# Optimization experiments

Hardware: AMD Instinct MI355X
Metric: run time of the kernel (lower is better)

Reference implementation:

```python
import jax, jax.numpy as jnp
import numpy as np

NHEAD = 8
TEMP = 1.0
LAMB = 1.0
G_MIN = 1e-3


def _linear(x, w, b):
    # torch nn.Linear convention: w is (out, in)
    return x @ w.T + b


def _ln(x, s, b):
    m = x.mean(-1, keepdims=True)
    v = ((x - m) ** 2).mean(-1, keepdims=True)
    return (x - m) / jnp.sqrt(v + 1e-5) * s + b


def _gate(x, w, b):
    # UncertaintyGate, gate_mode='mu_times_evi'
    nig = _linear(x, w, b)  # [B, L, 4]
    mu = nig[..., 0]
    v = jax.nn.softplus(nig[..., 1]) + 1e-6
    alpha = jax.nn.softplus(nig[..., 2]) + 1.0 + 1e-6
    beta = jax.nn.softplus(nig[..., 3]) + 1e-6
    sigma_e2 = beta / (v * (alpha - 1.0))
    g = jax.nn.sigmoid(mu) * jnp.exp(-LAMB * sigma_e2)
    return jnp.clip(g, G_MIN, 1.0)  # [B, L]


def _cross_attn(q, k, v, gate, mask):
    B, Lq, D = q.shape
    Lk = k.shape[1]
    hd = D // NHEAD
    q = q.reshape(B, Lq, NHEAD, hd).transpose(0, 2, 1, 3)
    k = k.reshape(B, Lk, NHEAD, hd).transpose(0, 2, 1, 3)
    v = v.reshape(B, Lk, NHEAD, hd).transpose(0, 2, 1, 3)
    scores = jnp.einsum('bhqd,bhkd->bhqk', q, k) / jnp.sqrt(jnp.float32(hd))
    scores = scores + jnp.log(gate + 1e-9)[:, None, None, :]  # per-key log-gate bias
    scores = jnp.where(mask[:, None, None, :] == 0, -1e9, scores)
    attn = jax.nn.softmax(scores / TEMP, axis=-1)
    out = jnp.einsum('bhqk,bhkd->bhqd', attn, v)
    return out.transpose(0, 2, 1, 3).reshape(B, Lq, D)


def _ffn(x, w1, b1, w2, b2):
    return _linear(jax.nn.gelu(_linear(x, w1, b1), approximate=False), w2, b2)


def setup_inputs() -> dict:
    key = jax.random.key(0)
    ks = iter(jax.random.split(key, 64))
    D, B, Ld, Lp = 512, 16, 256, 1024
    def w(shape, s=0.02):
        return jax.random.normal(next(ks), shape, jnp.float32) * s
    inp = {
        'h_d': jax.random.normal(next(ks), (B, Ld, D), jnp.float32),
        'h_p': jax.random.normal(next(ks), (B, Lp, D), jnp.float32),
        'gd_w': w((4, D)), 'gd_b': jnp.zeros((4,), jnp.float32),
        'gp_w': w((4, D)), 'gp_b': jnp.zeros((4,), jnp.float32),
        'wqd_w': w((D, D)), 'wqd_b': jnp.zeros((D,), jnp.float32),
        'wkp_w': w((D, D)), 'wkp_b': jnp.zeros((D,), jnp.float32),
        'wvp_w': w((D, D)), 'wvp_b': jnp.zeros((D,), jnp.float32),
        'wqp_w': w((D, D)), 'wqp_b': jnp.zeros((D,), jnp.float32),
        'wkd_w': w((D, D)), 'wkd_b': jnp.zeros((D,), jnp.float32),
        'wvd_w': w((D, D)), 'wvd_b': jnp.zeros((D,), jnp.float32),
        'od_w': w((D, D)), 'od_b': jnp.zeros((D,), jnp.float32),
        'op_w': w((D, D)), 'op_b': jnp.zeros((D,), jnp.float32),
        'fd1_w': w((4 * D, D)), 'fd1_b': jnp.zeros((4 * D,), jnp.float32),
        'fd2_w': w((D, 4 * D)), 'fd2_b': jnp.zeros((D,), jnp.float32),
        'fp1_w': w((4 * D, D)), 'fp1_b': jnp.zeros((4 * D,), jnp.float32),
        'fp2_w': w((D, 4 * D)), 'fp2_b': jnp.zeros((D,), jnp.float32),
        'nd1_s': jnp.ones((D,), jnp.float32), 'nd1_b': jnp.zeros((D,), jnp.float32),
        'nd2_s': jnp.ones((D,), jnp.float32), 'nd2_b': jnp.zeros((D,), jnp.float32),
        'np1_s': jnp.ones((D,), jnp.float32), 'np1_b': jnp.zeros((D,), jnp.float32),
        'np2_s': jnp.ones((D,), jnp.float32), 'np2_b': jnp.zeros((D,), jnp.float32),
        'mask_d': jnp.ones((B, Ld), jnp.int32),
        'mask_p': jnp.ones((B, Lp), jnp.int32),
    }
    return inp


def reference(h_d, h_p, gd_w, gd_b, gp_w, gp_b, wqd_w, wqd_b, wkp_w, wkp_b,
              wvp_w, wvp_b, wqp_w, wqp_b, wkd_w, wkd_b, wvd_w, wvd_b,
              od_w, od_b, op_w, op_b, fd1_w, fd1_b, fd2_w, fd2_b,
              fp1_w, fp1_b, fp2_w, fp2_b, nd1_s, nd1_b, nd2_s, nd2_b,
              np1_s, np1_b, np2_s, np2_b, mask_d, mask_p):
    # gates are computed from the ORIGINAL inputs
    g_d = _gate(h_d, gd_w, gd_b)
    g_p = _gate(h_p, gp_w, gp_b)
    # drug attends to protein
    attn_d = _cross_attn(_linear(h_d, wqd_w, wqd_b),
                         _linear(h_p, wkp_w, wkp_b),
                         _linear(h_p, wvp_w, wvp_b), g_p, mask_p)
    h_d = _ln(h_d + _linear(attn_d, od_w, od_b), nd1_s, nd1_b)
    # protein attends to UPDATED drug (matches original control flow)
    attn_p = _cross_attn(_linear(h_p, wqp_w, wqp_b),
                         _linear(h_d, wkd_w, wkd_b),
                         _linear(h_d, wvd_w, wvd_b), g_d, mask_d)
    h_p = _ln(h_p + _linear(attn_p, op_w, op_b), np1_s, np1_b)
    h_d = _ln(h_d + _ffn(h_d, fd1_w, fd1_b, fd2_w, fd2_b), nd2_s, nd2_b)
    h_p = _ln(h_p + _ffn(h_p, fp1_w, fp1_b, fp2_w, fp2_b), np2_s, np2_b)
    return (h_d, h_p)
```

## Files before the change

kernel.cpp:

```cpp
#include <hip/hip_runtime.h>

typedef float f32x4 __attribute__((ext_vector_type(4)));
typedef short bfrag __attribute__((ext_vector_type(8)));
typedef short s16x8 __attribute__((ext_vector_type(8)));
typedef unsigned short u16;

__device__ __forceinline__ u16 f2bf(float f) {
  union { float f; unsigned u; } x; x.f = f;
  unsigned r = x.u + 0x7fffu + ((x.u >> 16) & 1u);
  return (u16)(r >> 16);
}
__device__ __forceinline__ float bf2f(u16 v) {
  union { unsigned u; float f; } x; x.u = ((unsigned)v) << 16;
  return x.f;
}

__device__ __forceinline__ void g2l16(const void* g, void* l) {
  void* gnc = const_cast<void*>(g);
  __builtin_amdgcn_global_load_lds((__attribute__((address_space(1))) void*)gnc,
                                   (__attribute__((address_space(3))) void*)l, 16, 0, 0);
}

__device__ __forceinline__ f32x4 mfma16(bfrag a, bfrag b, f32x4 c) {
  asm volatile("v_mfma_f32_16x16x32_bf16 %0, %1, %2, %0" : "+v"(c) : "v"(a), "v"(b));
  return c;
}

__device__ __forceinline__ float wred_sum(float s) {
  #pragma unroll
  for (int o = 32; o; o >>= 1) s += __shfl_xor(s, o);
  return s;
}

__device__ __forceinline__ float gelu_f(float v) {
  return 0.5f * v * (1.f + erff(v * 0.70710678118f));
}

struct CvtArgs {
  const float* s[14];
  u16* d[14];
  int eb[14];
};

__global__ __launch_bounds__(256) void cvt_all(CvtArgs a) {
  const int blk = blockIdx.x;
  int base = 0;
  const float* sp = a.s[0];
  u16* dp = a.d[0];
  #pragma unroll
  for (int i = 0; i < 13; ++i) {
    if (blk >= a.eb[i]) { base = a.eb[i]; sp = a.s[i + 1]; dp = a.d[i + 1]; }
  }
  const size_t gi = ((size_t)(blk - base) * 256 + threadIdx.x) * 4;
  float4 f = *(const float4*)(sp + gi);
  ushort4 o;
  o.x = f2bf(f.x); o.y = f2bf(f.y); o.z = f2bf(f.z); o.w = f2bf(f.w);
  *(ushort4*)(dp + gi) = o;
}

__global__ __launch_bounds__(512) void biascat_k(
    const float* __restrict__ bkp, const float* __restrict__ bvp,
    const float* __restrict__ bqp, const float* __restrict__ bkd,
    const float* __restrict__ bvd, float* __restrict__ bp3,
    float* __restrict__ bd2) {
  int t = threadIdx.x;
  bp3[t] = bkp[t];
  bp3[512 + t] = bvp[t];
  bp3[1024 + t] = bqp[t];
  bd2[t] = bkd[t];
  bd2[512 + t] = bvd[t];
}

__device__ __forceinline__ float softplus_s(float x) {
  return fmaxf(x, 0.f) + log1pf(expf(-fabsf(x)));
}

__global__ __launch_bounds__(256) void gate_k(
    const float* __restrict__ hd, const float* __restrict__ hp,
    const float* __restrict__ wd, const float* __restrict__ bd,
    const float* __restrict__ wp, const float* __restrict__ bp,
    float* __restrict__ lgd, float* __restrict__ lgp, int mdTok) {
  const int lane = threadIdx.x & 63, wv = threadIdx.x >> 6;
  size_t tok = (size_t)blockIdx.x * 4 + wv;
  const float* h; const float* w4; const float* b4; float* lg;
  if (tok < (size_t)mdTok) { h = hd; w4 = wd; b4 = bd; lg = lgd; }
  else { h = hp; w4 = wp; b4 = bp; lg = lgp; tok -= mdTok; }
  const float* x = h + tok * 512;
  float s0 = 0.f, s1 = 0.f, s2 = 0.f, s3 = 0.f;
  #pragma unroll
  for (int i = 0; i < 8; ++i) {
    int c = (i << 6) + lane;
    float xv = x[c];
    s0 += xv * w4[c];
    s1 += xv * w4[512 + c];
    s2 += xv * w4[1024 + c];
    s3 += xv * w4[1536 + c];
  }
  s0 = wred_sum(s0); s1 = wred_sum(s1); s2 = wred_sum(s2); s3 = wred_sum(s3);
  if (lane == 0) {
    float mu = s0 + b4[0];
    float va = softplus_s(s1 + b4[1]) + 1e-6f;
    float al = softplus_s(s2 + b4[2]) + 1.f + 1e-6f;
    float be = softplus_s(s3 + b4[3]) + 1e-6f;
    float se2 = be / (va * (al - 1.f));
    float g = (1.f / (1.f + expf(-mu))) * expf(-se2);
    g = fminf(fmaxf(g, 1e-3f), 1.f);
    lg[tok] = logf(g + 1e-9f);
  }
}

__device__ __forceinline__ void ln_body(const u16* res, const u16* y,
                                        const float* sc, const float* bi,
                                        void* outv, int fp32out, size_t row,
                                        int lane) {
  const int c0 = lane * 8;
  float v[8];
  s16x8 yv = *(const s16x8*)(y + row * 512 + c0);
  s16x8 rv = *(const s16x8*)(res + row * 512 + c0);
  float s = 0.f;
  #pragma unroll
  for (int i = 0; i < 8; ++i) {
    v[i] = bf2f((u16)rv[i]) + bf2f((u16)yv[i]);
    s += v[i];
  }
  s = wred_sum(s);
  float m = s * (1.f / 512.f);
  float s2 = 0.f;
  #pragma unroll
  for (int i = 0; i < 8; ++i) { float d = v[i] - m; s2 += d * d; }
  s2 = wred_sum(s2);
  float inv = rsqrtf(s2 * (1.f / 512.f) + 1e-5f);
  float4 sc0 = *(const float4*)(sc + c0), sc1 = *(const float4*)(sc + c0 + 4);
  float4 bi0 = *(const float4*)(bi + c0), bi1 = *(const float4*)(bi + c0 + 4);
  float scv[8] = {sc0.x, sc0.y, sc0.z, sc0.w, sc1.x, sc1.y, sc1.z, sc1.w};
  float biv[8] = {bi0.x, bi0.y, bi0.z, bi0.w, bi1.x, bi1.y, bi1.z, bi1.w};
  float o[8];
  #pragma unroll
  for (int i = 0; i < 8; ++i) o[i] = (v[i] - m) * inv * scv[i] + biv[i];
  if (fp32out) {
    float* of = (float*)outv + row * 512 + c0;
    *(float4*)of = float4{o[0], o[1], o[2], o[3]};
    *(float4*)(of + 4) = float4{o[4], o[5], o[6], o[7]};
  } else {
    s16x8 ov;
    #pragma unroll
    for (int i = 0; i < 8; ++i) ov[i] = (short)f2bf(o[i]);
    *(s16x8*)((u16*)outv + row * 512 + c0) = ov;
  }
}

__global__ __launch_bounds__(256) void ln_k(const u16* __restrict__ res,
                                            const u16* __restrict__ y,
                                            const float* __restrict__ sc,
                                            const float* __restrict__ bi,
                                            u16* __restrict__ out) {
  const int lane = threadIdx.x & 63, w = threadIdx.x >> 6;
  const size_t row = (size_t)blockIdx.x * 4 + w;
  ln_body(res, y, sc, bi, out, 0, row, lane);
}

__global__ __launch_bounds__(256) void lnf_k(
    const u16* __restrict__ rd, const u16* __restrict__ yd,
    const float* __restrict__ scd, const float* __restrict__ bid,
    float* __restrict__ od,
    const u16* __restrict__ rp, const u16* __restrict__ yp,
    const float* __restrict__ scp, const float* __restrict__ bip,
    float* __restrict__ op, int mdRows) {
  const int lane = threadIdx.x & 63, w = threadIdx.x >> 6;
  size_t row = (size_t)blockIdx.x * 4 + w;
  if (row < (size_t)mdRows)
    ln_body(rd, yd, scd, bid, od, 1, row, lane);
  else
    ln_body(rp, yp, scp, bip, op, 1, row - mdRows, lane);
}

template <int KT>
__global__ __launch_bounds__(256) void flash_k(
    const u16* __restrict__ Q, const u16* __restrict__ Kv,
    const u16* __restrict__ Vt, const float* __restrict__ logg,
    const int* __restrict__ mask, u16* __restrict__ Out,
    int Lq, int Lk, float scale) {
  __shared__ __align__(16) u16 Kl[KT * 64];
  __shared__ __align__(16) u16 Vl[64 * KT];
  __shared__ __align__(16) u16 Pl[64 * (KT + 8)];
  const int tid = threadIdx.x;
  const int lane = tid & 63, wv = tid >> 6;
  const int lr = lane & 15, lg4 = lane >> 4;
  const int bh = blockIdx.z;
  const int b = bh >> 3, h = bh & 7;
  const int q0 = blockIdx.x * 64;

  bfrag af[2];
  {
    const u16* qrow = Q + (size_t)(b * Lq + q0 + wv * 16 + lr) * 512 + h * 64;
    af[0] = *(const bfrag*)(qrow + lg4 * 8);
    af[1] = *(const bfrag*)(qrow + 32 + lg4 * 8);
  }
  float mreg[4] = {-3e38f, -3e38f, -3e38f, -3e38f};
  float lreg[4] = {0.f, 0.f, 0.f, 0.f};
  f32x4 Oa[4] = {};
  const float* lgb = logg + (size_t)b * Lk;
  const int* mkb = mask + (size_t)b * Lk;

  const int NKT = Lk / KT;
  for (int t = 0; t < NKT; ++t) {
    const int k0 = t * KT;
    __syncthreads();
    {
      const char* kb = (const char*)(Kv + (size_t)(b * Lk + k0) * 512 + h * 64);
      #pragma unroll
      for (int r = 0; r < KT / 32; ++r) {
        int o = r * 4096 + tid * 16;
        int rr = o >> 7, cd = (o >> 4) & 7;
        int cs = cd ^ (rr & 7);
        g2l16(kb + (size_t)rr * 1024 + cs * 16, (char*)Kl + o);
      }
      const char* vb = (const char*)(Vt + (size_t)bh * 64 * Lk + k0);
      #pragma unroll
      for (int r = 0; r < KT / 32; ++r) {
        int o = r * 4096 + tid * 16;
        int rr = o >> 8, cd = (o >> 4) & 15;
        int cs = (cd & 8) | ((cd & 7) ^ (rr & 7));
        g2l16(vb + (size_t)rr * (Lk * 2) + cs * 16, (char*)Vl + o);
      }
    }
    __syncthreads();

    f32x4 sa[KT / 16];
    #pragma unroll
    for (int n = 0; n < KT / 16; ++n) {
      sa[n] = f32x4{0.f, 0.f, 0.f, 0.f};
      int row = n * 16 + lr;
      #pragma unroll
      for (int ks = 0; ks < 2; ++ks) {
        bfrag kf = *(const bfrag*)(Kl + row * 64 + (((ks * 4 + lg4) ^ (row & 7)) * 8));
        sa[n] = mfma16(af[ks], kf, sa[n]);
      }
    }
    asm volatile("s_nop 7\n\ts_nop 7");

    float pv[KT / 16][4];
    float nm[4] = {-3e38f, -3e38f, -3e38f, -3e38f};
    #pragma unroll
    for (int n = 0; n < KT / 16; ++n) {
      int kk = k0 + n * 16 + lr;
      float lgv = lgb[kk];
      int mkv = mkb[kk];
      #pragma unroll
      for (int e = 0; e < 4; ++e) {
        float tv = mkv ? fmaf(sa[n][e], scale, lgv) : -1e9f;
        pv[n][e] = tv;
        nm[e] = fmaxf(nm[e], tv);
      }
    }
    float fac[4], rs[4];
    #pragma unroll
    for (int e = 0; e < 4; ++e) {
      nm[e] = fmaxf(nm[e], __shfl_xor(nm[e], 1));
      nm[e] = fmaxf(nm[e], __shfl_xor(nm[e], 2));
      nm[e] = fmaxf(nm[e], __shfl_xor(nm[e], 4));
      nm[e] = fmaxf(nm[e], __shfl_xor(nm[e], 8));
      nm[e] = fmaxf(nm[e], mreg[e]);
      fac[e] = __expf(mreg[e] - nm[e]);
      mreg[e] = nm[e];
      rs[e] = 0.f;
    }
    #pragma unroll
    for (int n = 0; n < KT / 16; ++n)
      #pragma unroll
      for (int e = 0; e < 4; ++e) {
        float p = __expf(pv[n][e] - nm[e]);
        pv[n][e] = p;
        rs[e] += p;
      }
    #pragma unroll
    for (int e = 0; e < 4; ++e) {
      rs[e] += __shfl_xor(rs[e], 1);
      rs[e] += __shfl_xor(rs[e], 2);
      rs[e] += __shfl_xor(rs[e], 4);
      rs[e] += __shfl_xor(rs[e], 8);
      lreg[e] = lreg[e] * fac[e] + rs[e];
    }
    #pragma unroll
    for (int n2 = 0; n2 < 4; ++n2)
      #pragma unroll
      for (int e = 0; e < 4; ++e) Oa[n2][e] *= fac[e];

    {
      int prow = wv * 16 + lg4 * 4;
      #pragma unroll
      for (int n = 0; n < KT / 16; ++n)
        #pragma unroll
        for (int e = 0; e < 4; ++e)
          Pl[(prow + e) * (KT + 8) + n * 16 + lr] = f2bf(pv[n][e]);
    }
    #pragma unroll
    for (int ks = 0; ks < KT / 32; ++ks) {
      bfrag pf = *(const bfrag*)(Pl + (wv * 16 + lr) * (KT + 8) + (ks * 4 + lg4) * 8);
      #pragma unroll
      for (int n2 = 0; n2 < 4; ++n2) {
        int vrow = n2 * 16 + lr;
        int ch = ks * 4 + lg4;
        int chs = (ch & 8) | ((ch & 7) ^ (vrow & 7));
        bfrag vf = *(const bfrag*)(Vl + vrow * KT + chs * 8);
        Oa[n2] = mfma16(pf, vf, Oa[n2]);
      }
    }
  }
  asm volatile("s_nop 7\n\ts_nop 7");

  float inv[4];
  #pragma unroll
  for (int e = 0; e < 4; ++e) inv[e] = 1.f / lreg[e];
  u16* ob = Out + (size_t)(b * Lq + q0 + wv * 16 + lg4 * 4) * 512 + h * 64;
  #pragma unroll
  for (int n2 = 0; n2 < 4; ++n2)
    #pragma unroll
    for (int e = 0; e < 4; ++e)
      ob[(size_t)e * 512 + n2 * 16 + lr] = f2bf(Oa[n2][e] * inv[e]);
}

struct GemmDesc {
  const u16* A;
  const u16* W;
  const float* bias;
  u16 *C, *C2, *C3;
  int K, lda, ldw, ldc, NB, TR, epi, nblocks;
};

__global__ __launch_bounds__(256) void gemm_k(GemmDesc d0, GemmDesc d1) {
  __shared__ __align__(16) u16 Al[128 * 32];
  __shared__ __align__(16) u16 Wl[128 * 32];
  const int tid = threadIdx.x;
  const int qq = gridDim.x >> 3;
  int wg = (blockIdx.x & 7) * qq + (blockIdx.x >> 3);
  const GemmDesc& d = (wg < d0.nblocks) ? d0 : d1;
  if (wg >= d0.nblocks) wg -= d0.nblocks;
  const int bx = wg % d.NB, by = wg / d.NB;
  const int row0 = by * 128, col0 = bx * 128;
  const int lane = tid & 63, wv = tid >> 6;
  const int wr = wv >> 1, wc = wv & 1;
  const int rowW = wr * 64, colW = wc * 64;
  const int lr = lane & 15, lg4 = lane >> 4;
  const int K = d.K;

  const u16* aSrc[2];
  const u16* wSrc[2];
  int aDst[2], wDst[2];
  #pragma unroll
  for (int r = 0; r < 2; ++r) {
    int o = r * 4096 + tid * 16;
    int row = o >> 6, cd = (o >> 4) & 3, cs = cd ^ ((row >> 1) & 3);
    aSrc[r] = d.A + (size_t)(row0 + row) * d.lda + cs * 8;
    wSrc[r] = d.W + (size_t)(col0 + row) * d.ldw + cs * 8;
    aDst[r] = o;
    wDst[r] = o;
  }
  int aOff[4], wOff[4];
  #pragma unroll
  for (int m = 0; m < 4; ++m) {
    int rowi = rowW + m * 16 + lr;
    aOff[m] = rowi * 32 + ((lg4 ^ ((rowi >> 1) & 3)) * 8);
    int rowj = colW + m * 16 + lr;
    wOff[m] = rowj * 32 + ((lg4 ^ ((rowj >> 1) & 3)) * 8);
  }

  f32x4 acc[4][4] = {};

  for (int k0 = 0; k0 < K; k0 += 32) {
    #pragma unroll
    for (int r = 0; r < 2; ++r) g2l16(aSrc[r] + k0, (char*)Al + aDst[r]);
    #pragma unroll
    for (int r = 0; r < 2; ++r) g2l16(wSrc[r] + k0, (char*)Wl + wDst[r]);
    __syncthreads();
    bfrag af[4], wf[4];
    #pragma unroll
    for (int m = 0; m < 4; ++m) af[m] = *(const bfrag*)(Al + aOff[m]);
    #pragma unroll
    for (int n = 0; n < 4; ++n) wf[n] = *(const bfrag*)(Wl + wOff[n]);
    #pragma unroll
    for (int m = 0; m < 4; ++m)
      #pragma unroll
      for (int n = 0; n < 4; ++n) acc[m][n] = mfma16(af[m], wf[n], acc[m][n]);
    if (k0 + 32 < K) __syncthreads();
  }
  asm volatile("s_nop 7\n\ts_nop 7\n\ts_nop 7");

  #pragma unroll
  for (int m = 0; m < 4; ++m) {
    #pragma unroll
    for (int n = 0; n < 4; ++n) {
      int rb = row0 + rowW + m * 16 + lg4 * 4;
      int c = col0 + colW + n * 16 + lr;
      float bv = d.bias[c];
      if (d.epi == 1) {
        #pragma unroll
        for (int e = 0; e < 4; ++e)
          d.C[(size_t)(rb + e) * d.ldc + c] = f2bf(acc[m][n][e] + bv);
      } else if (d.epi == 2) {
        #pragma unroll
        for (int e = 0; e < 4; ++e)
          d.C[(size_t)(rb + e) * d.ldc + c] = f2bf(gelu_f(acc[m][n][e] + bv));
      } else if (d.epi == 4) {
        if (c < 512) {
          #pragma unroll
          for (int e = 0; e < 4; ++e)
            d.C[(size_t)(rb + e) * 512 + c] = f2bf(acc[m][n][e] + bv);
        } else if (c < 1024) {
          int cl = c - 512;
          int b2 = rb / d.TR, j0 = rb - b2 * d.TR;
          int h2 = cl >> 6, dd = cl & 63;
          ushort4 pk;
          pk.x = f2bf(acc[m][n][0] + bv);
          pk.y = f2bf(acc[m][n][1] + bv);
          pk.z = f2bf(acc[m][n][2] + bv);
          pk.w = f2bf(acc[m][n][3] + bv);
          *(ushort4*)&d.C2[(((size_t)b2 * 8 + h2) * 64 + dd) * d.TR + j0] = pk;
        } else {
          int cl = c - 1024;
          #pragma unroll
          for (int e = 0; e < 4; ++e)
            d.C3[(size_t)(rb + e) * 512 + cl] = f2bf(acc[m][n][e] + bv);
        }
      } else {
        if (c < 512) {
          #pragma unroll
          for (int e = 0; e < 4; ++e)
            d.C[(size_t)(rb + e) * d.ldc + c] = f2bf(acc[m][n][e] + bv);
        } else {
          int cl = c - 512;
          int b2 = rb / d.TR, j0 = rb - b2 * d.TR;
          int h2 = cl >> 6, dd = cl & 63;
          ushort4 pk;
          pk.x = f2bf(acc[m][n][0] + bv);
          pk.y = f2bf(acc[m][n][1] + bv);
          pk.z = f2bf(acc[m][n][2] + bv);
          pk.w = f2bf(acc[m][n][3] + bv);
          *(ushort4*)&d.C2[(((size_t)b2 * 8 + h2) * 64 + dd) * d.TR + j0] = pk;
        }
      }
    }
  }
}

extern "C" void kernel_launch(void* const* d_in, const int* in_sizes, int n_in,
                              void* d_out, int out_size, void* d_ws, size_t ws_size,
                              hipStream_t stream) {
  const float* h_d = (const float*)d_in[0];
  const float* h_p = (const float*)d_in[1];
  const float* gd_w = (const float*)d_in[2];
  const float* gd_b = (const float*)d_in[3];
  const float* gp_w = (const float*)d_in[4];
  const float* gp_b = (const float*)d_in[5];
  const float* wqd_w = (const float*)d_in[6];  const float* wqd_b = (const float*)d_in[7];
  const float* wkp_w = (const float*)d_in[8];  const float* wkp_b = (const float*)d_in[9];
  const float* wvp_w = (const float*)d_in[10]; const float* wvp_b = (const float*)d_in[11];
  const float* wqp_w = (const float*)d_in[12]; const float* wqp_b = (const float*)d_in[13];
  const float* wkd_w = (const float*)d_in[14]; const float* wkd_b = (const float*)d_in[15];
  const float* wvd_w = (const float*)d_in[16]; const float* wvd_b = (const float*)d_in[17];
  const float* od_w = (const float*)d_in[18];  const float* od_b = (const float*)d_in[19];
  const float* op_w = (const float*)d_in[20];  const float* op_b = (const float*)d_in[21];
  const float* fd1_w = (const float*)d_in[22]; const float* fd1_b = (const float*)d_in[23];
  const float* fd2_w = (const float*)d_in[24]; const float* fd2_b = (const float*)d_in[25];
  const float* fp1_w = (const float*)d_in[26]; const float* fp1_b = (const float*)d_in[27];
  const float* fp2_w = (const float*)d_in[28]; const float* fp2_b = (const float*)d_in[29];
  const float* nd1_s = (const float*)d_in[30]; const float* nd1_b = (const float*)d_in[31];
  const float* nd2_s = (const float*)d_in[32]; const float* nd2_b = (const float*)d_in[33];
  const float* np1_s = (const float*)d_in[34]; const float* np1_b = (const float*)d_in[35];
  const float* np2_s = (const float*)d_in[36]; const float* np2_b = (const float*)d_in[37];
  const int* mask_d = (const int*)d_in[38];
  const int* mask_p = (const int*)d_in[39];

  constexpr int B = 16, Ld = 256, Lp = 1024, D = 512, H = 8, F = 2048;
  constexpr int Md = B * Ld;
  constexpr int Mp = B * Lp;
  constexpr int BH = B * H;

  char* ws = (char*)d_ws;
  size_t off = 0;
  auto alloc = [&](size_t bytes) {
    size_t o = off;
    off += (bytes + 255) & ~(size_t)255;
    return o;
  };
  auto a16 = [&](size_t els) { return (u16*)(ws + alloc(els * 2)); };
  auto a32 = [&](size_t els) { return (float*)(ws + alloc(els * 4)); };

  u16* w_qd = a16((size_t)D * D);
  u16* w_kp = a16((size_t)D * D);
  u16* w_vp = a16((size_t)D * D);
  u16* w_qp = a16((size_t)D * D);
  u16* w_kd = a16((size_t)D * D);
  u16* w_vd = a16((size_t)D * D);
  u16* w_od = a16((size_t)D * D);
  u16* w_op = a16((size_t)D * D);
  u16* w_fd1 = a16((size_t)F * D);
  u16* w_fd2 = a16((size_t)F * D);
  u16* w_fp1 = a16((size_t)F * D);
  u16* w_fp2 = a16((size_t)F * D);

  u16* hd16 = a16((size_t)Md * D);
  u16* hd2_16 = a16((size_t)Md * D);
  u16* hp16 = a16((size_t)Mp * D);
  u16* qd16 = a16((size_t)Md * D);
  u16* kp16 = a16((size_t)Mp * D);
  u16* qp16 = a16((size_t)Mp * D);
  u16* vt16 = a16((size_t)Mp * D);
  u16* obuf16 = a16((size_t)Mp * D);
  u16* obuf_d = a16((size_t)Md * D);
  u16* t16 = a16((size_t)Mp * F);
  u16* t16d = a16((size_t)Md * F);
  float* logg_d = a32(Md);
  float* logg_p = a32(Mp);
  float* bp3 = a32(1536);
  float* bd2 = a32(1024);

  {
    CvtArgs a;
    const float* src[14] = {h_d, h_p, wqd_w, wkp_w, wvp_w, wqp_w, wkd_w,
                            wvd_w, od_w, op_w, fd1_w, fd2_w, fp1_w, fp2_w};
    u16* dst[14] = {hd16, hp16, w_qd, w_kp, w_vp, w_qp, w_kd,
                    w_vd, w_od, w_op, w_fd1, w_fd2, w_fp1, w_fp2};
    const int nelem[14] = {Md * D, Mp * D, D * D, D * D, D * D, D * D, D * D,
                           D * D, D * D, D * D, F * D, F * D, F * D, F * D};
    int pfx = 0;
    for (int i = 0; i < 14; ++i) {
      a.s[i] = src[i];
      a.d[i] = dst[i];
      pfx += nelem[i] / 1024;
      a.eb[i] = pfx;
    }
    cvt_all<<<pfx, 256, 0, stream>>>(a);
  }
  biascat_k<<<1, 512, 0, stream>>>(wkp_b, wvp_b, wqp_b, wkd_b, wvd_b, bp3, bd2);

  gate_k<<<(Md + Mp) / 4, 256, 0, stream>>>(h_d, h_p, gd_w, gd_b, gp_w, gp_b,
                                            logg_d, logg_p, Md);

  GemmDesc none = {};

  {
    GemmDesc kvq = {hp16, w_kp, bp3, kp16, vt16, qp16,
                    D, D, D, D, 1536 / 128, Lp, 4, (Mp / 128) * (1536 / 128)};
    GemmDesc qd = {hd16, w_qd, wqd_b, qd16, nullptr, nullptr,
                   D, D, D, D, D / 128, 0, 1, (Md / 128) * (D / 128)};
    gemm_k<<<kvq.nblocks + qd.nblocks, 256, 0, stream>>>(kvq, qd);
  }

  flash_k<128><<<dim3(Ld / 64, 1, BH), 256, 0, stream>>>(
      qd16, kp16, vt16, logg_p, mask_p, qd16, Ld, Lp, 0.125f);

  {
    GemmDesc od = {qd16, w_od, od_b, obuf_d, nullptr, nullptr,
                   D, D, D, D, D / 128, 0, 1, (Md / 128) * (D / 128)};
    gemm_k<<<od.nblocks, 256, 0, stream>>>(od, none);
  }
  ln_k<<<Md / 4, 256, 0, stream>>>(hd16, obuf_d, nd1_s, nd1_b, hd2_16);

  {
    GemmDesc kdvd = {hd2_16, w_kd, bd2, qd16, vt16, nullptr,
                     D, D, D, D, 1024 / 128, Ld, 5, (Md / 128) * (1024 / 128)};
    GemmDesc fd1 = {hd2_16, w_fd1, fd1_b, t16d, nullptr, nullptr,
                    D, D, D, F, F / 128, 0, 2, (Md / 128) * (F / 128)};
    gemm_k<<<kdvd.nblocks + fd1.nblocks, 256, 0, stream>>>(kdvd, fd1);
  }

  flash_k<128><<<dim3(Lp / 64, 1, BH), 256, 0, stream>>>(
      qp16, qd16, vt16, logg_d, mask_d, qp16, Lp, Ld, 0.125f);

  {
    GemmDesc op = {qp16, w_op, op_b, obuf16, nullptr, nullptr,
                   D, D, D, D, D / 128, 0, 1, (Mp / 128) * (D / 128)};
    gemm_k<<<op.nblocks, 256, 0, stream>>>(op, none);
  }
  ln_k<<<Mp / 4, 256, 0, stream>>>(hp16, obuf16, np1_s, np1_b, hp16);

  {
    GemmDesc fp1 = {hp16, w_fp1, fp1_b, t16, nullptr, nullptr,
                    D, D, D, F, F / 128, 0, 2, (Mp / 128) * (F / 128)};
    GemmDesc fd2 = {t16d, w_fd2, fd2_b, obuf_d, nullptr, nullptr,
                    F, F, F, D, D / 128, 0, 1, (Md / 128) * (D / 128)};
    gemm_k<<<fp1.nblocks + fd2.nblocks, 256, 0, stream>>>(fp1, fd2);
  }

  {
    GemmDesc fp2 = {t16, w_fp2, fp2_b, obuf16, nullptr, nullptr,
                    F, F, F, D, D / 128, 0, 1, (Mp / 128) * (D / 128)};
    gemm_k<<<fp2.nblocks, 256, 0, stream>>>(fp2, none);
  }

  lnf_k<<<(Md + Mp) / 4, 256, 0, stream>>>(
      hd2_16, obuf_d, nd2_s, nd2_b, (float*)d_out,
      hp16, obuf16, np2_s, np2_b, (float*)d_out + (size_t)Md * D, Md);
}
```

Baseline: 422.1 us.

## Template GEMM on tile sizes with K-step 64, XCD swizzle, and regrouped launches

The GEMM kernel becomes a template over block tile and thread count. It stages 64-wide K slices per barrier instead of 32, with a new 8-way XOR LDS swizzle, and remaps workgroups so contiguous tiles land on the same XCD. The large-M GEMMs (KVQ projection, FFN1 on the protein side) use 256x128 tiles with 512 threads for more reuse per block, and fd2 is now paired with fp2 instead of fp1. Costs are more LDS per block and fewer, larger blocks, which can lower occupancy or leave CUs idle on the tail. Bigger tiles could also misbehave if Md is not divisible by 256, though here it is.

```diff
diff --git a/kernel.cpp b/kernel.cpp
--- a/kernel.cpp
+++ b/kernel.cpp
@@ -328,61 +328,80 @@
   int K, lda, ldw, ldc, NB, TR, epi, nblocks;
 };
 
-__global__ __launch_bounds__(256) void gemm_k(GemmDesc d0, GemmDesc d1) {
-  __shared__ __align__(16) u16 Al[128 * 32];
-  __shared__ __align__(16) u16 Wl[128 * 32];
+__device__ __forceinline__ int xcdswz(int wg, int nb) {
+  int xcd = wg & 7, idx = wg >> 3, q = nb >> 3, r = nb & 7;
+  return (xcd < r ? xcd * (q + 1) : r * (q + 1) + (xcd - r) * q) + idx;
+}
+
+template <int BM, int BN, int NTHR>
+__global__ __launch_bounds__(NTHR) void gemm_t(GemmDesc d0, GemmDesc d1) {
+  __shared__ __align__(16) u16 Al[BM * 64];
+  __shared__ __align__(16) u16 Wl[BN * 64];
   const int tid = threadIdx.x;
-  const int qq = gridDim.x >> 3;
-  int wg = (blockIdx.x & 7) * qq + (blockIdx.x >> 3);
+  int wg = blockIdx.x;
   const GemmDesc& d = (wg < d0.nblocks) ? d0 : d1;
   if (wg >= d0.nblocks) wg -= d0.nblocks;
+  wg = xcdswz(wg, d.nblocks);
   const int bx = wg % d.NB, by = wg / d.NB;
-  const int row0 = by * 128, col0 = bx * 128;
+  const int row0 = by * BM, col0 = bx * BN;
   const int lane = tid & 63, wv = tid >> 6;
-  const int wr = wv >> 1, wc = wv & 1;
+  const int wr = wv / (BN / 64), wc = wv % (BN / 64);
   const int rowW = wr * 64, colW = wc * 64;
   const int lr = lane & 15, lg4 = lane >> 4;
-  const int K = d.K;
-
-  const u16* aSrc[2];
-  const u16* wSrc[2];
-  int aDst[2], wDst[2];
-  #pragma unroll
-  for (int r = 0; r < 2; ++r) {
-    int o = r * 4096 + tid * 16;
-    int row = o >> 6, cd = (o >> 4) & 3, cs = cd ^ ((row >> 1) & 3);
+
+  constexpr int AR = BM * 128 / (NTHR * 16);
+  constexpr int WR = BN * 128 / (NTHR * 16);
+  const u16* aSrc[AR];
+  const u16* wSrc[WR];
+  int aDst[AR], wDst[WR];
+  #pragma unroll
+  for (int r = 0; r < AR; ++r) {
+    int o = r * (NTHR * 16) + tid * 16;
+    int row = o >> 7, cd = (o >> 4) & 7, cs = cd ^ (row & 7);
     aSrc[r] = d.A + (size_t)(row0 + row) * d.lda + cs * 8;
+    aDst[r] = o;
+  }
+  #pragma unroll
+  for (int r = 0; r < WR; ++r) {
+    int o = r * (NTHR * 16) + tid * 16;
+    int row = o >> 7, cd = (o >> 4) & 7, cs = cd ^ (row & 7);
     wSrc[r] = d.W + (size_t)(col0 + row) * d.ldw + cs * 8;
-    aDst[r] = o;
     wDst[r] = o;
   }
-  int aOff[4], wOff[4];
+  int aOff[4][2], wOff[4][2];
   #pragma unroll
   for (int m = 0; m < 4; ++m) {
     int rowi = rowW + m * 16 + lr;
-    aOff[m] = rowi * 32 + ((lg4 ^ ((rowi >> 1) & 3)) * 8);
     int rowj = colW + m * 16 + lr;
-    wOff[m] = rowj * 32 + ((lg4 ^ ((rowj >> 1) & 3)) * 8);
+    #pragma unroll
+    for (int ks = 0; ks < 2; ++ks) {
+      aOff[m][ks] = rowi * 64 + (((ks * 4 + lg4) ^ (rowi & 7)) * 8);
+      wOff[m][ks] = rowj * 64 + (((ks * 4 + lg4) ^ (rowj & 7)) * 8);
+    }
   }
 
   f32x4 acc[4][4] = {};
-
-  for (int k0 = 0; k0 < K; k0 += 32) {
-    #pragma unroll
-    for (int r = 0; r < 2; ++r) g2l16(aSrc[r] + k0, (char*)Al + aDst[r]);
-    #pragma unroll
-    for (int r = 0; r < 2; ++r) g2l16(wSrc[r] + k0, (char*)Wl + wDst[r]);
+  const int K = d.K;
+
+  for (int k0 = 0; k0 < K; k0 += 64) {
+    #pragma unroll
+    for (int r = 0; r < AR; ++r) g2l16(aSrc[r] + k0, (char*)Al + aDst[r]);
+    #pragma unroll
+    for (int r = 0; r < WR; ++r) g2l16(wSrc[r] + k0, (char*)Wl + wDst[r]);
     __syncthreads();
-    bfrag af[4], wf[4];
-    #pragma unroll
-    for (int m = 0; m < 4; ++m) af[m] = *(const bfrag*)(Al + aOff[m]);
-    #pragma unroll
-    for (int n = 0; n < 4; ++n) wf[n] = *(const bfrag*)(Wl + wOff[n]);
-    #pragma unroll
-    for (int m = 0; m < 4; ++m)
-      #pragma unroll
-      for (int n = 0; n < 4; ++n) acc[m][n] = mfma16(af[m], wf[n], acc[m][n]);
-    if (k0 + 32 < K) __syncthreads();
+    #pragma unroll
+    for (int ks = 0; ks < 2; ++ks) {
+      bfrag af[4], wf[4];
+      #pragma unroll
+      for (int m = 0; m < 4; ++m) af[m] = *(const bfrag*)(Al + aOff[m][ks]);
+      #pragma unroll
+      for (int n = 0; n < 4; ++n) wf[n] = *(const bfrag*)(Wl + wOff[n][ks]);
+      #pragma unroll
+      for (int m = 0; m < 4; ++m)
+        #pragma unroll
+        for (int n = 0; n < 4; ++n) acc[m][n] = mfma16(af[m], wf[n], acc[m][n]);
+    }
+    if (k0 + 64 < K) __syncthreads();
   }
   asm volatile("s_nop 7\n\ts_nop 7\n\ts_nop 7");
 
@@ -541,10 +560,10 @@
 
   {
     GemmDesc kvq = {hp16, w_kp, bp3, kp16, vt16, qp16,
-                    D, D, D, D, 1536 / 128, Lp, 4, (Mp / 128) * (1536 / 128)};
+                    D, D, D, D, 1536 / 128, Lp, 4, (Mp / 256) * (1536 / 128)};
     GemmDesc qd = {hd16, w_qd, wqd_b, qd16, nullptr, nullptr,
-                   D, D, D, D, D / 128, 0, 1, (Md / 128) * (D / 128)};
-    gemm_k<<<kvq.nblocks + qd.nblocks, 256, 0, stream>>>(kvq, qd);
+                   D, D, D, D, D / 128, 0, 1, (Md / 256) * (D / 128)};
+    gemm_t<256, 128, 512><<<kvq.nblocks + qd.nblocks, 512, 0, stream>>>(kvq, qd);
   }
 
   flash_k<128><<<dim3(Ld / 64, 1, BH), 256, 0, stream>>>(
@@ -553,7 +572,7 @@
   {
     GemmDesc od = {qd16, w_od, od_b, obuf_d, nullptr, nullptr,
                    D, D, D, D, D / 128, 0, 1, (Md / 128) * (D / 128)};
-    gemm_k<<<od.nblocks, 256, 0, stream>>>(od, none);
+    gemm_t<128, 128, 256><<<od.nblocks, 256, 0, stream>>>(od, none);
   }
   ln_k<<<Md / 4, 256, 0, stream>>>(hd16, obuf_d, nd1_s, nd1_b, hd2_16);
 
@@ -562,7 +581,7 @@
                      D, D, D, D, 1024 / 128, Ld, 5, (Md / 128) * (1024 / 128)};
     GemmDesc fd1 = {hd2_16, w_fd1, fd1_b, t16d, nullptr, nullptr,
                     D, D, D, F, F / 128, 0, 2, (Md / 128) * (F / 128)};
-    gemm_k<<<kdvd.nblocks + fd1.nblocks, 256, 0, stream>>>(kdvd, fd1);
+    gemm_t<128, 128, 256><<<kdvd.nblocks + fd1.nblocks, 256, 0, stream>>>(kdvd, fd1);
   }
 
   flash_k<128><<<dim3(Lp / 64, 1, BH), 256, 0, stream>>>(
@@ -571,22 +590,22 @@
   {
     GemmDesc op = {qp16, w_op, op_b, obuf16, nullptr, nullptr,
                    D, D, D, D, D / 128, 0, 1, (Mp / 128) * (D / 128)};
-    gemm_k<<<op.nblocks, 256, 0, stream>>>(op, none);
+    gemm_t<128, 128, 256><<<op.nblocks, 256, 0, stream>>>(op, none);
   }
   ln_k<<<Mp / 4, 256, 0, stream>>>(hp16, obuf16, np1_s, np1_b, hp16);
 
   {
     GemmDesc fp1 = {hp16, w_fp1, fp1_b, t16, nullptr, nullptr,
-                    D, D, D, F, F / 128, 0, 2, (Mp / 128) * (F / 128)};
+                    D, D, D, F, F / 128, 0, 2, (Mp / 256) * (F / 128)};
+    gemm_t<256, 128, 512><<<fp1.nblocks, 512, 0, stream>>>(fp1, none);
+  }
+
+  {
+    GemmDesc fp2 = {t16, w_fp2, fp2_b, obuf16, nullptr, nullptr,
+                    F, F, F, D, D / 128, 0, 1, (Mp / 128) * (D / 128)};
     GemmDesc fd2 = {t16d, w_fd2, fd2_b, obuf_d, nullptr, nullptr,
                     F, F, F, D, D / 128, 0, 1, (Md / 128) * (D / 128)};
-    gemm_k<<<fp1.nblocks + fd2.nblocks, 256, 0, stream>>>(fp1, fd2);
-  }
-
-  {
-    GemmDesc fp2 = {t16, w_fp2, fp2_b, obuf16, nullptr, nullptr,
-                    F, F, F, D, D / 128, 0, 1, (Mp / 128) * (D / 128)};
-    gemm_k<<<fp2.nblocks, 256, 0, stream>>>(fp2, none);
+    gemm_t<128, 128, 256><<<fp2.nblocks + fd2.nblocks, 256, 0, stream>>>(fp2, fd2);
   }
 
   lnf_k<<<(Md + Mp) / 4, 256, 0, stream>>>(
```

New measurement: 455.8 us. +8.0%, slower.

## Fuse activation bf16 conversion into gate kernel and deepen GEMM K-tile

Applied to the files above, without the earlier changes.

The fp32-to-bf16 conversion of h_d and h_p moves out of the bulk convert kernel and into the gate kernel, which already reads those activations, so they are read from global memory once instead of twice. The GEMM kernel's K-step grows from 32 to 64 with a wider 8-way XOR LDS swizzle, halving the number of barrier pairs per tile at the cost of doubled shared memory. The XCD block remapping becomes a per-descriptor swizzle that handles block counts not divisible by 8. Gate kernel stores are 2-byte scalar writes, which may coalesce less well than the old vectorised convert.

```diff
diff --git a/kernel.cpp b/kernel.cpp
--- a/kernel.cpp
+++ b/kernel.cpp
@@ -37,9 +37,9 @@
 }
 
 struct CvtArgs {
-  const float* s[14];
-  u16* d[14];
-  int eb[14];
+  const float* s[12];
+  u16* d[12];
+  int eb[12];
 };
 
 __global__ __launch_bounds__(256) void cvt_all(CvtArgs a) {
@@ -48,7 +48,7 @@
   const float* sp = a.s[0];
   u16* dp = a.d[0];
   #pragma unroll
-  for (int i = 0; i < 13; ++i) {
+  for (int i = 0; i < 11; ++i) {
     if (blk >= a.eb[i]) { base = a.eb[i]; sp = a.s[i + 1]; dp = a.d[i + 1]; }
   }
   const size_t gi = ((size_t)(blk - base) * 256 + threadIdx.x) * 4;
@@ -79,18 +79,21 @@
     const float* __restrict__ hd, const float* __restrict__ hp,
     const float* __restrict__ wd, const float* __restrict__ bd,
     const float* __restrict__ wp, const float* __restrict__ bp,
-    float* __restrict__ lgd, float* __restrict__ lgp, int mdTok) {
+    float* __restrict__ lgd, float* __restrict__ lgp,
+    u16* __restrict__ hd16, u16* __restrict__ hp16, int mdTok) {
   const int lane = threadIdx.x & 63, wv = threadIdx.x >> 6;
   size_t tok = (size_t)blockIdx.x * 4 + wv;
-  const float* h; const float* w4; const float* b4; float* lg;
-  if (tok < (size_t)mdTok) { h = hd; w4 = wd; b4 = bd; lg = lgd; }
-  else { h = hp; w4 = wp; b4 = bp; lg = lgp; tok -= mdTok; }
+  const float* h; const float* w4; const float* b4; float* lg; u16* ho;
+  if (tok < (size_t)mdTok) { h = hd; w4 = wd; b4 = bd; lg = lgd; ho = hd16; }
+  else { h = hp; w4 = wp; b4 = bp; lg = lgp; ho = hp16; tok -= mdTok; }
   const float* x = h + tok * 512;
+  u16* xo = ho + tok * 512;
   float s0 = 0.f, s1 = 0.f, s2 = 0.f, s3 = 0.f;
   #pragma unroll
   for (int i = 0; i < 8; ++i) {
     int c = (i << 6) + lane;
     float xv = x[c];
+    xo[c] = f2bf(xv);
     s0 += xv * w4[c];
     s1 += xv * w4[512 + c];
     s2 += xv * w4[1024 + c];
@@ -328,61 +331,72 @@
   int K, lda, ldw, ldc, NB, TR, epi, nblocks;
 };
 
+__device__ __forceinline__ int xcdswz(int wg, int nb) {
+  int xcd = wg & 7, idx = wg >> 3, q = nb >> 3, r = nb & 7;
+  return (xcd < r ? xcd * (q + 1) : r * (q + 1) + (xcd - r) * q) + idx;
+}
+
 __global__ __launch_bounds__(256) void gemm_k(GemmDesc d0, GemmDesc d1) {
-  __shared__ __align__(16) u16 Al[128 * 32];
-  __shared__ __align__(16) u16 Wl[128 * 32];
+  __shared__ __align__(16) u16 Al[128 * 64];
+  __shared__ __align__(16) u16 Wl[128 * 64];
   const int tid = threadIdx.x;
-  const int qq = gridDim.x >> 3;
-  int wg = (blockIdx.x & 7) * qq + (blockIdx.x >> 3);
+  int wg = blockIdx.x;
   const GemmDesc& d = (wg < d0.nblocks) ? d0 : d1;
   if (wg >= d0.nblocks) wg -= d0.nblocks;
+  wg = xcdswz(wg, d.nblocks);
   const int bx = wg % d.NB, by = wg / d.NB;
   const int row0 = by * 128, col0 = bx * 128;
   const int lane = tid & 63, wv = tid >> 6;
   const int wr = wv >> 1, wc = wv & 1;
   const int rowW = wr * 64, colW = wc * 64;
   const int lr = lane & 15, lg4 = lane >> 4;
-  const int K = d.K;
-
-  const u16* aSrc[2];
-  const u16* wSrc[2];
-  int aDst[2], wDst[2];
-  #pragma unroll
-  for (int r = 0; r < 2; ++r) {
+
+  const u16* aSrc[4];
+  const u16* wSrc[4];
+  int aDst[4], wDst[4];
+  #pragma unroll
+  for (int r = 0; r < 4; ++r) {
     int o = r * 4096 + tid * 16;
-    int row = o >> 6, cd = (o >> 4) & 3, cs = cd ^ ((row >> 1) & 3);
+    int row = o >> 7, cd = (o >> 4) & 7, cs = cd ^ (row & 7);
     aSrc[r] = d.A + (size_t)(row0 + row) * d.lda + cs * 8;
     wSrc[r] = d.W + (size_t)(col0 + row) * d.ldw + cs * 8;
     aDst[r] = o;
     wDst[r] = o;
   }
-  int aOff[4], wOff[4];
+  int aOff[4][2], wOff[4][2];
   #pragma unroll
   for (int m = 0; m < 4; ++m) {
     int rowi = rowW + m * 16 + lr;
-    aOff[m] = rowi * 32 + ((lg4 ^ ((rowi >> 1) & 3)) * 8);
     int rowj = colW + m * 16 + lr;
-    wOff[m] = rowj * 32 + ((lg4 ^ ((rowj >> 1) & 3)) * 8);
+    #pragma unroll
+    for (int ks = 0; ks < 2; ++ks) {
+      aOff[m][ks] = rowi * 64 + (((ks * 4 + lg4) ^ (rowi & 7)) * 8);
+      wOff[m][ks] = rowj * 64 + (((ks * 4 + lg4) ^ (rowj & 7)) * 8);
+    }
   }
 
   f32x4 acc[4][4] = {};
-
-  for (int k0 = 0; k0 < K; k0 += 32) {
-    #pragma unroll
-    for (int r = 0; r < 2; ++r) g2l16(aSrc[r] + k0, (char*)Al + aDst[r]);
-    #pragma unroll
-    for (int r = 0; r < 2; ++r) g2l16(wSrc[r] + k0, (char*)Wl + wDst[r]);
+  const int K = d.K;
+
+  for (int k0 = 0; k0 < K; k0 += 64) {
+    #pragma unroll
+    for (int r = 0; r < 4; ++r) g2l16(aSrc[r] + k0, (char*)Al + aDst[r]);
+    #pragma unroll
+    for (int r = 0; r < 4; ++r) g2l16(wSrc[r] + k0, (char*)Wl + wDst[r]);
     __syncthreads();
-    bfrag af[4], wf[4];
-    #pragma unroll
-    for (int m = 0; m < 4; ++m) af[m] = *(const bfrag*)(Al + aOff[m]);
-    #pragma unroll
-    for (int n = 0; n < 4; ++n) wf[n] = *(const bfrag*)(Wl + wOff[n]);
-    #pragma unroll
-    for (int m = 0; m < 4; ++m)
-      #pragma unroll
-      for (int n = 0; n < 4; ++n) acc[m][n] = mfma16(af[m], wf[n], acc[m][n]);
-    if (k0 + 32 < K) __syncthreads();
+    #pragma unroll
+    for (int ks = 0; ks < 2; ++ks) {
+      bfrag af[4], wf[4];
+      #pragma unroll
+      for (int m = 0; m < 4; ++m) af[m] = *(const bfrag*)(Al + aOff[m][ks]);
+      #pragma unroll
+      for (int n = 0; n < 4; ++n) wf[n] = *(const bfrag*)(Wl + wOff[n][ks]);
+      #pragma unroll
+      for (int m = 0; m < 4; ++m)
+        #pragma unroll
+        for (int n = 0; n < 4; ++n) acc[m][n] = mfma16(af[m], wf[n], acc[m][n]);
+    }
+    if (k0 + 64 < K) __syncthreads();
   }
   asm volatile("s_nop 7\n\ts_nop 7\n\ts_nop 7");
 
@@ -517,14 +531,14 @@
 
   {
     CvtArgs a;
-    const float* src[14] = {h_d, h_p, wqd_w, wkp_w, wvp_w, wqp_w, wkd_w,
-                            wvd_w, od_w, op_w, fd1_w, fd2_w, fp1_w, fp2_w};
-    u16* dst[14] = {hd16, hp16, w_qd, w_kp, w_vp, w_qp, w_kd,
-                    w_vd, w_od, w_op, w_fd1, w_fd2, w_fp1, w_fp2};
-    const int nelem[14] = {Md * D, Mp * D, D * D, D * D, D * D, D * D, D * D,
-                           D * D, D * D, D * D, F * D, F * D, F * D, F * D};
+    const float* src[12] = {wqd_w, wkp_w, wvp_w, wqp_w, wkd_w, wvd_w,
+                            od_w, op_w, fd1_w, fd2_w, fp1_w, fp2_w};
+    u16* dst[12] = {w_qd, w_kp, w_vp, w_qp, w_kd, w_vd,
+                    w_od, w_op, w_fd1, w_fd2, w_fp1, w_fp2};
+    const int nelem[12] = {D * D, D * D, D * D, D * D, D * D, D * D,
+                           D * D, D * D, F * D, F * D, F * D, F * D};
     int pfx = 0;
-    for (int i = 0; i < 14; ++i) {
+    for (int i = 0; i < 12; ++i) {
       a.s[i] = src[i];
       a.d[i] = dst[i];
       pfx += nelem[i] / 1024;
@@ -535,7 +549,7 @@
   biascat_k<<<1, 512, 0, stream>>>(wkp_b, wvp_b, wqp_b, wkd_b, wvd_b, bp3, bd2);
 
   gate_k<<<(Md + Mp) / 4, 256, 0, stream>>>(h_d, h_p, gd_w, gd_b, gp_w, gp_b,
-                                            logg_d, logg_p, Md);
+                                            logg_d, logg_p, hd16, hp16, Md);
 
   GemmDesc none = {};
 
```

Measured after the change: 375.4 us. 11.1% less time.
